# Performance work log

Measured on AMD Instinct MI355X. Metric: run time of the kernel, lower is better.

The kernel has to match this reference:

```python
import jax, jax.numpy as jnp
import numpy as np

S, B, D = 1024, 32, 1024

def setup_inputs() -> dict:
    key = jax.random.key(0)
    k1, k2, k3, k4, k5 = jax.random.split(key, 5)
    x = jax.random.normal(k1, (S, B, D), dtype=jnp.float32)
    layer_input = jax.random.normal(k2, (S, B, D), dtype=jnp.float32)
    position_embedding = jax.random.normal(k3, (S, B, D), dtype=jnp.float32)
    # pad indicator == 1 (True); random pads, ~half the positions
    encoder_mask = jax.random.randint(k4, (B, S), 0, 2).astype(bool)
    W = jax.random.normal(k5, (D, 1), dtype=jnp.float32) * (1.0 / np.sqrt(D))
    b = jnp.zeros((1,), dtype=jnp.float32)
    return {"x": x, "layer_input": layer_input,
            "position_embedding": position_embedding,
            "encoder_mask": encoder_mask, "W": W, "b": b}

def reference(x, layer_input, position_embedding, encoder_mask, W, b):
    s, bsz, d = x.shape
    valid = (~encoder_mask).astype(x.dtype)            # (B, S)
    sentence_length = valid.sum(axis=-1)               # (B,)
    langtok_index = s - sentence_length                # (B,)
    # predicted soft position in [0, sentence_length]
    pred = jax.nn.sigmoid(x @ W + b)[..., 0]           # (S, B)
    pred = pred * sentence_length[None, :]             # (S, B)
    # absolute positions shifted by language-token offset
    all_pos = jnp.arange(s, dtype=x.dtype)[:, None] - langtok_index[None, :]  # (S, B)
    # distances[i, b, j] = pred[i, b] - all_pos[j, b]
    dist = pred[:, :, None] - all_pos.T[None, :, :]    # (S, B, S)
    prob = 1.0 / (dist * dist + 0.001)                 # reciprocal squared distance
    prob = prob * valid[None, :, :]                    # zero out pads along j
    prob = prob / prob.sum(axis=-1, keepdims=True)     # normalize over source positions
    # weighted sum of position embeddings: (S,B,S) x (S,B,D) -> (S,B,D)
    out = jnp.einsum('ibj,jbd->ibd', prob, position_embedding)
    out = out * valid.T[:, :, None]                    # zero out pad rows
    return out
```

## Files before the change

kernel.cpp:

```cpp
#include <hip/hip_runtime.h>


#define S_ 1024
#define B_ 32
#define D_ 1024

typedef unsigned short us;
typedef __attribute__((ext_vector_type(4))) unsigned short us4;
typedef __attribute__((ext_vector_type(4))) float f4;
typedef __attribute__((ext_vector_type(8))) short short8;

__device__ __forceinline__ float bf2f(us u){
  unsigned v = ((unsigned)u) << 16;
  float f;
  __builtin_memcpy(&f, &v, 4);
  return f;
}
__device__ __forceinline__ us f2bf(float f){
  unsigned v;
  __builtin_memcpy(&v, &f, 4);
  v = v + 0x7fffu + ((v >> 16) & 1u);
  return (us)(v >> 16);
}

__device__ __forceinline__ void gll16(const void* g, void* l){
  __builtin_amdgcn_global_load_lds(
      (const __attribute__((address_space(1))) void*)g,
      (__attribute__((address_space(3))) void*)l,
      16, 0, 0);
}

__global__ __launch_bounds__(256) void prep_k(const unsigned char* __restrict__ mask,
                                              float* __restrict__ valid,
                                              float* __restrict__ slen,
                                              float* __restrict__ ltok)
{
  const int b = blockIdx.x;
  const int t = threadIdx.x;
  __shared__ int flags[5];
  __shared__ int red[256];
  if (t < 5) flags[t] = 0;
  __syncthreads();
  for (int k = 0; k < 32; ++k){
    int p = t * 32 + k;
    unsigned v = mask[p];
    if (v){
      atomicOr(&flags[p & 3], 1);
      if (v > 1u) atomicOr(&flags[4], 1);
    }
  }
  __syncthreads();
  int fmt;
  int any123 = flags[1] | flags[2] | flags[3];
  if (!flags[4]) fmt = any123 ? 0 : 1;
  else           fmt = (flags[0] | flags[1]) ? 2 : 3;

  int cnt = 0;
#pragma unroll
  for (int q = 0; q < 4; ++q){
    int j = t + q * 256;
    size_t idx = (size_t)b * S_ + j;
    unsigned mv;
    if (fmt == 0)      mv = mask[idx];
    else if (fmt == 1) mv = ((const unsigned int*)mask)[idx];
    else if (fmt == 2) mv = ((const unsigned short*)mask)[idx];
    else               mv = ((const unsigned int*)mask)[idx] & 0x7fffffffu;
    valid[idx] = mv ? 0.0f : 1.0f;
    cnt += mv ? 0 : 1;
  }
  red[t] = cnt;
  __syncthreads();
  for (int s = 128; s > 0; s >>= 1){
    if (t < s) red[t] += red[t + s];
    __syncthreads();
  }
  if (t == 0){
    float cn = (float)red[0];
    slen[b] = cn;
    ltok[b] = (float)S_ - cn;
  }
}

__global__ __launch_bounds__(256) void transp_k(const float* __restrict__ pe,
                                                us* __restrict__ Etr)
{
  __shared__ us tile[64 * 68];
  const int id = blockIdx.x;
  const int j0 = (id & 15) * 64;
  const int d0 = ((id >> 4) & 15) * 64;
  const int b  = id >> 8;

  const int t  = threadIdx.x;
  const int rr = t >> 4, cc = t & 15;
#pragma unroll
  for (int q = 0; q < 4; ++q){
    int j = q * 16 + rr;
    float4 v = *(const float4*)(pe + ((size_t)(j0 + j) * B_ + b) * D_ + d0 + cc * 4);
    us4 tv; tv.x = f2bf(v.x); tv.y = f2bf(v.y); tv.z = f2bf(v.z); tv.w = f2bf(v.w);
    *(us4*)&tile[j * 68 + cc * 4] = tv;
  }
  __syncthreads();
#pragma unroll
  for (int q = 0; q < 4; ++q){
    int d = q * 16 + rr;
    us4 v;
    v.x = tile[(cc * 4 + 0) * 68 + d];
    v.y = tile[(cc * 4 + 1) * 68 + d];
    v.z = tile[(cc * 4 + 2) * 68 + d];
    v.w = tile[(cc * 4 + 3) * 68 + d];
    *(us4*)(Etr + ((size_t)b * D_ + d0 + d) * S_ + j0 + cc * 4) = v;
  }
}

__global__ __launch_bounds__(256) void rowk_k(const float* __restrict__ x,
                                              const float* __restrict__ Wp,
                                              const float* __restrict__ bp,
                                              const float* __restrict__ valid,
                                              const float* __restrict__ slen,
                                              const float* __restrict__ ltok,
                                              us* __restrict__ P,
                                              float* __restrict__ rs,
                                              float* __restrict__ c_arr)
{
  const int wid  = threadIdx.x >> 6;
  const int lane = threadIdx.x & 63;
  const int row  = blockIdx.x * 4 + wid;
  const int b = row & (B_ - 1);
  const int i = row >> 5;

  const float4* xr = (const float4*)(x + (size_t)row * D_);
  const float4* wr = (const float4*)Wp;
  float acc = 0.f;
#pragma unroll
  for (int q = 0; q < 4; ++q){
    float4 xv = xr[q * 64 + lane];
    float4 wv = wr[q * 64 + lane];
    acc += xv.x * wv.x + xv.y * wv.y + xv.z * wv.z + xv.w * wv.w;
  }
#pragma unroll
  for (int off = 32; off > 0; off >>= 1) acc += __shfl_xor(acc, off);

  float z   = acc + bp[0];
  float sig = 1.f / (1.f + expf(-z));
  float c   = sig * slen[b] + ltok[b];

  const float4* vr = (const float4*)(valid + (size_t)b * S_);
  us4* Pr = (us4*)(P + ((size_t)b * S_ + i) * S_);
  float wsum = 0.f;
#pragma unroll
  for (int q = 0; q < 4; ++q){
    int idx = q * 64 + lane;
    float4 vv = vr[idx];
    float j0 = (float)(idx * 4);
    float d0 = c - j0;
    float d1 = c - (j0 + 1.f);
    float d2 = c - (j0 + 2.f);
    float d3 = c - (j0 + 3.f);
    us p0 = f2bf(vv.x * __builtin_amdgcn_rcpf(d0 * d0 + 1e-3f));
    us p1 = f2bf(vv.y * __builtin_amdgcn_rcpf(d1 * d1 + 1e-3f));
    us p2 = f2bf(vv.z * __builtin_amdgcn_rcpf(d2 * d2 + 1e-3f));
    us p3 = f2bf(vv.w * __builtin_amdgcn_rcpf(d3 * d3 + 1e-3f));
    us4 pv; pv.x = p0; pv.y = p1; pv.z = p2; pv.w = p3;
    Pr[idx] = pv;
    wsum += bf2f(p0) + bf2f(p1) + bf2f(p2) + bf2f(p3);
  }
#pragma unroll
  for (int off = 32; off > 0; off >>= 1) wsum += __shfl_xor(wsum, off);

  if (lane == 0){
    float vi = valid[(size_t)b * S_ + i];
    rs[(size_t)b * S_ + i] = (vi != 0.f) ? (vi / wsum) : 0.f;
    c_arr[(size_t)b * S_ + i] = c;
  }
}

__global__ __launch_bounds__(512, 2) void gemm_k(const us* __restrict__ P,
                                                 const us* __restrict__ Etr,
                                                 const float* __restrict__ rs,
                                                 float* __restrict__ out)
{
  const int bid = blockIdx.x;
  const int xcd = bid & 7;
  const int s   = bid >> 3;
  const int b   = xcd * 4 + (s >> 4);
  const int t16 = s & 15;
  const int i0  = (t16 >> 2) * 256;
  const int n0  = (t16 & 3) * 256;

  const int tid  = threadIdx.x;
  const int wid  = tid >> 6;
  const int lane = tid & 63;
  const int wm = wid >> 2, wn = wid & 3;
  const int ml = lane & 15, quad = lane >> 4;

  __shared__ __align__(16) us lds[4][2][8192];

  const us* gsrc[2];
  {
    int p = tid;
    int r = p >> 2;
    int c = (p & 3) ^ ((r >> 1) & 3);
    gsrc[0] = P   + ((size_t)b * S_ + (i0 + r)) * S_ + c * 8;
    gsrc[1] = Etr + ((size_t)b * D_ + (n0 + r)) * S_ + c * 8;
  }
  const int dst0 = wid * 64 * 8;

  int aoff[8], boff[4];
#pragma unroll
  for (int mt = 0; mt < 8; ++mt){
    int r = wm * 128 + mt * 16 + ml;
    aoff[mt] = r * 32 + ((quad ^ ((r >> 1) & 3)) * 8);
  }
#pragma unroll
  for (int nt = 0; nt < 4; ++nt){
    int r = wn * 64 + nt * 16 + ml;
    boff[nt] = r * 32 + ((quad ^ ((r >> 1) & 3)) * 8);
  }

  f4 acc[8][4];
#pragma unroll
  for (int mt = 0; mt < 8; ++mt)
#pragma unroll
    for (int nt = 0; nt < 4; ++nt){
      f4 z = {0.0f, 0.0f, 0.0f, 0.0f};
      acc[mt][nt] = z;
    }

  auto STAGE = [&](int slot, int kt){
    const us* gA = gsrc[0] + kt * 32;
    const us* gB = gsrc[1] + kt * 32;
    us* lA = &lds[slot][0][dst0];
    us* lB = &lds[slot][1][dst0];
    gll16(gA,            lA);
    gll16(gA + 128 * S_, lA + 4096);
    gll16(gB,            lB);
    gll16(gB + 128 * S_, lB + 4096);
  };
  auto READF = [&](short8* f, int slot){
    const us* A  = lds[slot][0];
    const us* Bm = lds[slot][1];
#pragma unroll
    for (int mt = 0; mt < 8; ++mt) f[mt] = *(const short8*)&A[aoff[mt]];
#pragma unroll
    for (int nt = 0; nt < 4; ++nt) f[8 + nt] = *(const short8*)&Bm[boff[nt]];
  };
  auto MFMA32 = [&](const short8* f){
    __builtin_amdgcn_s_setprio(1);
#pragma unroll
    for (int mt = 0; mt < 8; ++mt)
#pragma unroll
      for (int nt = 0; nt < 4; ++nt)
        acc[mt][nt] = __builtin_amdgcn_mfma_f32_16x16x32_bf16(f[mt], f[8 + nt], acc[mt][nt], 0, 0, 0);
    __builtin_amdgcn_s_setprio(0);
  };
  short8 fA[12], fB[12];
  auto HALF = [&](int kt, short8* cur, short8* nxt){
    asm volatile("s_waitcnt vmcnt(4)" ::: "memory");
    asm volatile("s_waitcnt lgkmcnt(0)" ::: "memory");
    __builtin_amdgcn_sched_barrier(0);
    __builtin_amdgcn_s_barrier();
    const int ktn = (kt + 3 < 32) ? (kt + 3) : 31;
    STAGE((kt + 3) & 3, ktn);
    READF(nxt, (kt + 1) & 3);
    MFMA32(cur);
  };

  STAGE(0, 0); STAGE(1, 1); STAGE(2, 2);
  asm volatile("s_waitcnt vmcnt(8)" ::: "memory");
  __builtin_amdgcn_s_barrier();
  READF(fA, 0);

#pragma unroll 1
  for (int kt = 0; kt < 32; kt += 2){
    HALF(kt,     fA, fB);
    HALF(kt + 1, fB, fA);
  }
  asm volatile("s_waitcnt vmcnt(0)" ::: "memory");

  const float* rsb = rs + (size_t)b * S_;
#pragma unroll
  for (int mt = 0; mt < 8; ++mt){
#pragma unroll
    for (int reg = 0; reg < 4; ++reg){
      int i = i0 + wm * 128 + mt * 16 + quad * 4 + reg;
      float rv = rsb[i];
      size_t ob = ((size_t)i * B_ + b) * D_;
#pragma unroll
      for (int nt = 0; nt < 4; ++nt){
        int d = n0 + wn * 64 + nt * 16 + ml;
        out[ob + d] = acc[mt][nt][reg] * rv;
      }
    }
  }
}

__global__ __launch_bounds__(256) void rowk_nb(const float* __restrict__ x,
                                               const float* __restrict__ Wp,
                                               const float* __restrict__ bp,
                                               const float* __restrict__ valid,
                                               const float* __restrict__ slen,
                                               const float* __restrict__ ltok,
                                               float* __restrict__ rs,
                                               float* __restrict__ c_arr)
{
  const int wid  = threadIdx.x >> 6;
  const int lane = threadIdx.x & 63;
  const int row  = blockIdx.x * 4 + wid;
  const int b = row & (B_ - 1);
  const int i = row >> 5;

  const float4* xr = (const float4*)(x + (size_t)row * D_);
  const float4* wr = (const float4*)Wp;
  float acc = 0.f;
#pragma unroll
  for (int q = 0; q < 4; ++q){
    float4 xv = xr[q * 64 + lane];
    float4 wv = wr[q * 64 + lane];
    acc += xv.x * wv.x + xv.y * wv.y + xv.z * wv.z + xv.w * wv.w;
  }
#pragma unroll
  for (int off = 32; off > 0; off >>= 1) acc += __shfl_xor(acc, off);

  float z   = acc + bp[0];
  float sig = 1.f / (1.f + expf(-z));
  float c   = sig * slen[b] + ltok[b];

  const float4* vr = (const float4*)(valid + (size_t)b * S_);
  float wsum = 0.f;
#pragma unroll
  for (int q = 0; q < 4; ++q){
    int idx = q * 64 + lane;
    float4 vv = vr[idx];
    float j0 = (float)(idx * 4);
    float d0 = c - j0;
    float d1 = c - (j0 + 1.f);
    float d2 = c - (j0 + 2.f);
    float d3 = c - (j0 + 3.f);
    us p0 = f2bf(vv.x / (d0 * d0 + 1e-3f));
    us p1 = f2bf(vv.y / (d1 * d1 + 1e-3f));
    us p2 = f2bf(vv.z / (d2 * d2 + 1e-3f));
    us p3 = f2bf(vv.w / (d3 * d3 + 1e-3f));
    wsum += bf2f(p0) + bf2f(p1) + bf2f(p2) + bf2f(p3);
  }
#pragma unroll
  for (int off = 32; off > 0; off >>= 1) wsum += __shfl_xor(wsum, off);

  if (lane == 0){
    float vi = valid[(size_t)b * S_ + i];
    rs[(size_t)b * S_ + i] = (vi != 0.f) ? (vi / wsum) : 0.f;
    c_arr[(size_t)b * S_ + i] = c;
  }
}

__global__ __launch_bounds__(256) void slow_out_k(const float* __restrict__ pe,
                                                  const float* __restrict__ valid,
                                                  const float* __restrict__ c_arr,
                                                  const float* __restrict__ rs,
                                                  float* __restrict__ out)
{
  const int bid = blockIdx.x;
  const int b = bid & (B_ - 1);
  const int i = bid >> 5;
  const int t = threadIdx.x;
  __shared__ float sw[S_];
  float c  = c_arr[(size_t)b * S_ + i];
  float rv = rs[(size_t)b * S_ + i];
#pragma unroll
  for (int q = 0; q < 4; ++q){
    int j = t + q * 256;
    float d = c - (float)j;
    sw[j] = valid[(size_t)b * S_ + j] / (d * d + 1e-3f);
  }
  __syncthreads();
  float a0 = 0, a1 = 0, a2 = 0, a3 = 0;
  if (rv != 0.0f){
    for (int j = 0; j < S_; ++j){
      float wj = sw[j];
      const float* row = pe + ((size_t)j * B_ + b) * D_;
      a0 += wj * row[t];
      a1 += wj * row[t + 256];
      a2 += wj * row[t + 512];
      a3 += wj * row[t + 768];
    }
  }
  float* orow = out + ((size_t)i * B_ + b) * D_;
  orow[t]       = a0 * rv;
  orow[t + 256] = a1 * rv;
  orow[t + 512] = a2 * rv;
  orow[t + 768] = a3 * rv;
}

extern "C" void kernel_launch(void* const* d_in, const int* in_sizes, int n_in,
                              void* d_out, int out_size, void* d_ws, size_t ws_size,
                              hipStream_t stream)
{
  (void)in_sizes; (void)n_in; (void)out_size;
  const float* x  = (const float*)d_in[0];
  const float* pe = (const float*)d_in[2];
  const unsigned char* mask = (const unsigned char*)d_in[3];
  const float* Wp = (const float*)d_in[4];
  const float* bp = (const float*)d_in[5];
  float* out = (float*)d_out;
  char* ws = (char*)d_ws;

  const size_t offValid = 0;
  const size_t offRs    = offValid + (size_t)B_ * S_ * 4;
  const size_t offSlen  = offRs    + (size_t)B_ * S_ * 4;
  const size_t offLtok  = offSlen  + 128;
  const size_t offC     = offLtok  + 128;
  const size_t offP     = offC     + (size_t)B_ * S_ * 4;
  const size_t offE     = offP     + (size_t)B_ * S_ * S_ * 2;
  const size_t need     = offE     + (size_t)B_ * D_ * S_ * 2;

  float* valid = (float*)(ws + offValid);
  float* rs    = (float*)(ws + offRs);
  float* slen  = (float*)(ws + offSlen);
  float* ltok  = (float*)(ws + offLtok);
  float* c_arr = (float*)(ws + offC);
  us* P   = (us*)(ws + offP);
  us* Etr = (us*)(ws + offE);

  prep_k<<<B_, 256, 0, stream>>>(mask, valid, slen, ltok);
  if (ws_size >= need){
    transp_k<<<8192, 256, 0, stream>>>(pe, Etr);
    rowk_k<<<S_ * B_ / 4, 256, 0, stream>>>(x, Wp, bp, valid, slen, ltok, P, rs, c_arr);
    gemm_k<<<512, 512, 0, stream>>>(P, Etr, rs, out);
  } else {
    rowk_nb<<<S_ * B_ / 4, 256, 0, stream>>>(x, Wp, bp, valid, slen, ltok, rs, c_arr);
    slow_out_k<<<S_ * B_, 256, 0, stream>>>(pe, valid, c_arr, rs, out);
  }
}
```

Measured before the change: 463.4 us.

## Widen transpose tiles and restructure GEMM main loop to single-buffered fragments

The transpose kernel now has each block handle four 64x64 d-tiles (256 d columns), so global loads read 1 KB contiguous rows per wavefront and the grid shrinks fourfold. The GEMM main loop drops the register double-buffered fragment scheme (fA/fB with lookahead LDS reads) and instead reads fragments for the current slot, issues the next stage load, and runs the MFMAs in two halves with an end-of-iteration wait and barrier. This lowers register pressure from 24 fragment registers to 12. The trade-off is less overlap of LDS reads with MFMA work.

Result: slower. 477.4 us (+3.0%).

```diff
diff --git a/kernel.cpp b/kernel.cpp
--- a/kernel.cpp
+++ b/kernel.cpp
@@ -84,31 +84,37 @@
 __global__ __launch_bounds__(256) void transp_k(const float* __restrict__ pe,
                                                 us* __restrict__ Etr)
 {
-  __shared__ us tile[64 * 68];
+  __shared__ us tile[4][64 * 68 + 8];
   const int id = blockIdx.x;
   const int j0 = (id & 15) * 64;
-  const int d0 = ((id >> 4) & 15) * 64;
-  const int b  = id >> 8;
+  const int d0 = ((id >> 4) & 3) * 256;
+  const int b  = id >> 6;
 
   const int t  = threadIdx.x;
-  const int rr = t >> 4, cc = t & 15;
-#pragma unroll
-  for (int q = 0; q < 4; ++q){
-    int j = q * 16 + rr;
+  const int rr = t >> 6, cc = t & 63;
+  const int ddw = cc >> 4;
+  const int c16 = cc & 15;
+#pragma unroll
+  for (int q = 0; q < 16; ++q){
+    int j = q * 4 + rr;
     float4 v = *(const float4*)(pe + ((size_t)(j0 + j) * B_ + b) * D_ + d0 + cc * 4);
     us4 tv; tv.x = f2bf(v.x); tv.y = f2bf(v.y); tv.z = f2bf(v.z); tv.w = f2bf(v.w);
-    *(us4*)&tile[j * 68 + cc * 4] = tv;
+    *(us4*)&tile[ddw][j * 68 + c16 * 4] = tv;
   }
   __syncthreads();
-#pragma unroll
-  for (int q = 0; q < 4; ++q){
-    int d = q * 16 + rr;
-    us4 v;
-    v.x = tile[(cc * 4 + 0) * 68 + d];
-    v.y = tile[(cc * 4 + 1) * 68 + d];
-    v.z = tile[(cc * 4 + 2) * 68 + d];
-    v.w = tile[(cc * 4 + 3) * 68 + d];
-    *(us4*)(Etr + ((size_t)b * D_ + d0 + d) * S_ + j0 + cc * 4) = v;
+  const int rr2 = t >> 4, cc2 = t & 15;
+#pragma unroll
+  for (int dd = 0; dd < 4; ++dd){
+#pragma unroll
+    for (int q = 0; q < 4; ++q){
+      int d = q * 16 + rr2;
+      us4 v;
+      v.x = tile[dd][(cc2 * 4 + 0) * 68 + d];
+      v.y = tile[dd][(cc2 * 4 + 1) * 68 + d];
+      v.z = tile[dd][(cc2 * 4 + 2) * 68 + d];
+      v.w = tile[dd][(cc2 * 4 + 3) * 68 + d];
+      *(us4*)(Etr + ((size_t)b * D_ + d0 + dd * 64 + d) * S_ + j0 + cc2 * 4) = v;
+    }
   }
 }
 
@@ -236,44 +242,49 @@
     gll16(gB,            lB);
     gll16(gB + 128 * S_, lB + 4096);
   };
-  auto READF = [&](short8* f, int slot){
-    const us* A  = lds[slot][0];
-    const us* Bm = lds[slot][1];
-#pragma unroll
-    for (int mt = 0; mt < 8; ++mt) f[mt] = *(const short8*)&A[aoff[mt]];
-#pragma unroll
-    for (int nt = 0; nt < 4; ++nt) f[8 + nt] = *(const short8*)&Bm[boff[nt]];
-  };
-  auto MFMA32 = [&](const short8* f){
-    __builtin_amdgcn_s_setprio(1);
-#pragma unroll
-    for (int mt = 0; mt < 8; ++mt)
-#pragma unroll
-      for (int nt = 0; nt < 4; ++nt)
-        acc[mt][nt] = __builtin_amdgcn_mfma_f32_16x16x32_bf16(f[mt], f[8 + nt], acc[mt][nt], 0, 0, 0);
-    __builtin_amdgcn_s_setprio(0);
-  };
-  short8 fA[12], fB[12];
-  auto HALF = [&](int kt, short8* cur, short8* nxt){
-    asm volatile("s_waitcnt vmcnt(4)" ::: "memory");
-    asm volatile("s_waitcnt lgkmcnt(0)" ::: "memory");
-    __builtin_amdgcn_sched_barrier(0);
-    __builtin_amdgcn_s_barrier();
-    const int ktn = (kt + 3 < 32) ? (kt + 3) : 31;
-    STAGE((kt + 3) & 3, ktn);
-    READF(nxt, (kt + 1) & 3);
-    MFMA32(cur);
-  };
-
-  STAGE(0, 0); STAGE(1, 1); STAGE(2, 2);
+
+  STAGE(0, 0);
+  STAGE(1, 1);
+  STAGE(2, 2);
   asm volatile("s_waitcnt vmcnt(8)" ::: "memory");
   __builtin_amdgcn_s_barrier();
-  READF(fA, 0);
+  asm volatile("" ::: "memory");
 
 #pragma unroll 1
-  for (int kt = 0; kt < 32; kt += 2){
-    HALF(kt,     fA, fB);
-    HALF(kt + 1, fB, fA);
+  for (int kt = 0; kt < 32; ++kt){
+    const int sl  = kt & 3;
+    const int st  = (kt + 3) & 3;
+    const int ktn = (kt < 29) ? (kt + 3) : 31;
+    const us* A = lds[sl][0];
+    const us* B = lds[sl][1];
+    short8 av[4], av2[4], bv[4];
+
+#pragma unroll
+    for (int mt = 0; mt < 4; ++mt) av[mt] = *(const short8*)&A[aoff[mt]];
+#pragma unroll
+    for (int nt = 0; nt < 4; ++nt) bv[nt] = *(const short8*)&B[boff[nt]];
+    STAGE(st, ktn);
+    __builtin_amdgcn_s_setprio(1);
+#pragma unroll
+    for (int mt = 0; mt < 4; ++mt)
+#pragma unroll
+      for (int nt = 0; nt < 4; ++nt)
+        acc[mt][nt] = __builtin_amdgcn_mfma_f32_16x16x32_bf16(av[mt], bv[nt], acc[mt][nt], 0, 0, 0);
+    __builtin_amdgcn_s_setprio(0);
+
+#pragma unroll
+    for (int mt = 0; mt < 4; ++mt) av2[mt] = *(const short8*)&A[aoff[4 + mt]];
+    __builtin_amdgcn_s_setprio(1);
+#pragma unroll
+    for (int mt = 0; mt < 4; ++mt)
+#pragma unroll
+      for (int nt = 0; nt < 4; ++nt)
+        acc[4 + mt][nt] = __builtin_amdgcn_mfma_f32_16x16x32_bf16(av2[mt], bv[nt], acc[4 + mt][nt], 0, 0, 0);
+    __builtin_amdgcn_s_setprio(0);
+
+    asm volatile("s_waitcnt vmcnt(8)" ::: "memory");
+    __builtin_amdgcn_s_barrier();
+    asm volatile("" ::: "memory");
   }
   asm volatile("s_waitcnt vmcnt(0)" ::: "memory");
 
@@ -422,7 +433,7 @@
 
   prep_k<<<B_, 256, 0, stream>>>(mask, valid, slen, ltok);
   if (ws_size >= need){
-    transp_k<<<8192, 256, 0, stream>>>(pe, Etr);
+    transp_k<<<2048, 256, 0, stream>>>(pe, Etr);
     rowk_k<<<S_ * B_ / 4, 256, 0, stream>>>(x, Wp, bp, valid, slen, ltok, P, rs, c_arr);
     gemm_k<<<512, 512, 0, stream>>>(P, Etr, rs, out);
   } else {
```
